# Kernel optimization log

Hardware: AMD Instinct MI355X
Metric: run time of the kernel (lower is better)

Reference implementation:

```python
import jax, jax.numpy as jnp
import numpy as np

NUM_HEADS = 16
HEAD_DIM = 128  # 2048 / 16


def setup_inputs() -> dict:
    key = jax.random.key(0)
    ks = jax.random.split(key, 5)
    B, S, D = 2, 2048, 2048
    scale = 1.0 / np.sqrt(D)
    return {
        "x": jax.random.normal(ks[0], (B, S, D), dtype=jnp.float32),
        "Wq": jax.random.normal(ks[1], (D, D), dtype=jnp.float32) * scale,
        "Wk": jax.random.normal(ks[2], (D, D), dtype=jnp.float32) * scale,
        "Wv": jax.random.normal(ks[3], (D, D), dtype=jnp.float32) * scale,
        "Wo": jax.random.normal(ks[4], (D, D), dtype=jnp.float32) * scale,
    }


def reference(x, Wq, Wk, Wv, Wo):
    B, S, D = x.shape
    H, Hd = NUM_HEADS, HEAD_DIM
    # nn.Linear(bias=False): y = x @ W.T
    q = (x @ Wq.T).reshape(B, S, H, Hd).transpose(0, 2, 1, 3)  # [B,H,S,Hd]
    k = (x @ Wk.T).reshape(B, S, H, Hd).transpose(0, 2, 1, 3)
    v = (x @ Wv.T).reshape(B, S, H, Hd).transpose(0, 2, 1, 3)
    scores = jnp.einsum("bhqd,bhkd->bhqk", q, k) / jnp.sqrt(jnp.float32(Hd))
    attn = jax.nn.softmax(scores, axis=-1)  # dropout p=0 (eval) -> identity
    out = jnp.einsum("bhqk,bhkd->bhqd", attn, v)  # [B,H,S,Hd]
    out = out.transpose(0, 2, 1, 3).reshape(B, S, D)
    out = out @ Wo.T
    return out
```

## Files before the change

### kernel.cpp

```cpp
#include <hip/hip_runtime.h>
#include <math.h>
#include <stdint.h>


#define DDIM 2048
#define SEQ  2048
#define NH   16
#define HD   128

typedef __attribute__((ext_vector_type(4))) float f32x4;
typedef __attribute__((ext_vector_type(16))) float f32x16;
typedef __attribute__((ext_vector_type(8))) __bf16 bf16x8;
typedef __attribute__((ext_vector_type(4))) unsigned int u32x4;
typedef __attribute__((ext_vector_type(2))) unsigned int u32x2;

#define MFMA_B16(a, b, c) __builtin_amdgcn_mfma_f32_16x16x32_bf16((a), (b), (c), 0, 0, 0)
#define MFMA32(a, b, c) __builtin_amdgcn_mfma_f32_32x32x16_bf16((a), (b), (c), 0, 0, 0)

__device__ __forceinline__ void async16(const void* g, void* l) {
  __builtin_amdgcn_global_load_lds(
      (const __attribute__((address_space(1))) unsigned int*)g,
      (__attribute__((address_space(3))) unsigned int*)l, 16, 0, 0);
}

__device__ __forceinline__ unsigned short f2bf(float f) {
  unsigned u = __builtin_bit_cast(unsigned, f);
  u += 0x7fffu + ((u >> 16) & 1u);
  return (unsigned short)(u >> 16);
}

__device__ __forceinline__ bf16x8 ldfrag(const unsigned short* p) {
  return __builtin_bit_cast(bf16x8, *(const u32x4*)p);
}

__device__ __forceinline__ void cvt_body(const float* __restrict__ s,
                                         unsigned short* __restrict__ d, int i) {
  const f32x4* sp = (const f32x4*)s;
  f32x4 a = sp[2 * i], b = sp[2 * i + 1];
  u32x4 o;
  o.x = ((unsigned)f2bf(a.y) << 16) | f2bf(a.x);
  o.y = ((unsigned)f2bf(a.w) << 16) | f2bf(a.z);
  o.z = ((unsigned)f2bf(b.y) << 16) | f2bf(b.x);
  o.w = ((unsigned)f2bf(b.w) << 16) | f2bf(b.z);
  ((u32x4*)d)[i] = o;
}

__global__ __launch_bounds__(256) void cvt_bf16_kernel(const float* __restrict__ s,
                                                       unsigned short* __restrict__ d) {
  cvt_body(s, d, blockIdx.x * 256 + threadIdx.x);
}

__global__ __launch_bounds__(256) void cvt_all_kernel(const float* __restrict__ x,
                                                      const float* __restrict__ wq,
                                                      const float* __restrict__ wk,
                                                      const float* __restrict__ wv,
                                                      const float* __restrict__ wo,
                                                      unsigned short* __restrict__ xb,
                                                      unsigned short* __restrict__ wqkv,
                                                      unsigned short* __restrict__ wob) {
  const int b = blockIdx.x;
  if (b < 4096) {
    cvt_body(x, xb, b * 256 + threadIdx.x);
  } else if (b < 10240) {
    const int wi = (b - 4096) >> 11, lb = (b - 4096) & 2047;
    const float* s = (wi == 0) ? wq : (wi == 1) ? wk : wv;
    cvt_body(s, wqkv + (size_t)wi * 4194304u, lb * 256 + threadIdx.x);
  } else {
    cvt_body(wo, wob, (b - 10240) * 256 + threadIdx.x);
  }
}

#define STG_A(NXT, HOFF, CB)                                              \
  {                                                                       \
    async16(pA[0] + (HOFF) * DDIM + (CB), &As[NXT][(HOFF) * 64 + tid * 8]); \
    async16(pA[1] + (HOFF) * DDIM + (CB),                                 \
            &As[NXT][(HOFF) * 64 + 4096 + tid * 8]);                      \
  }
#define STG_B(NXT, HOFF, CB)                                              \
  {                                                                       \
    async16(pB[0] + (HOFF) * DDIM + (CB), &Bs[NXT][(HOFF) * 64 + tid * 8]); \
    async16(pB[1] + (HOFF) * DDIM + (CB),                                 \
            &Bs[NXT][(HOFF) * 64 + 4096 + tid * 8]);                      \
  }
#define VM0 asm volatile("s_waitcnt vmcnt(0)" ::: "memory")
#define VMNONE (void)0

#define PHASE2(CUR, KS, STAGE_STMT, WAIT_STMT)                        \
  {                                                                   \
    const int ph = (KS) * 2 + half;                                   \
    bf16x8 af_[4], bf_[2];                                            \
    _Pragma("unroll") for (int mf = 0; mf < 4; ++mf) af_[mf] =        \
        ldfrag(&As[CUR][(wr * 128 + mf * 32 + l32) * 64 +             \
                        (ph ^ fr ^ ((mf & 1) * 4)) * 8]);             \
    _Pragma("unroll") for (int nf = 0; nf < 2; ++nf) bf_[nf] =        \
        ldfrag(&Bs[CUR][(wc * 64 + nf * 32 + l32) * 64 +              \
                        (ph ^ fr ^ (nf * 4)) * 8]);                   \
    STAGE_STMT;                                                       \
    __builtin_amdgcn_s_barrier();                                     \
    asm volatile("s_waitcnt lgkmcnt(0)" ::: "memory");                \
    __builtin_amdgcn_sched_barrier(0);                                \
    __builtin_amdgcn_s_setprio(1);                                    \
    _Pragma("unroll") for (int mf = 0; mf < 4; ++mf) {                \
      acc[mf][0] = MFMA32(af_[mf], bf_[0], acc[mf][0]);               \
      acc[mf][1] = MFMA32(af_[mf], bf_[1], acc[mf][1]);               \
    }                                                                 \
    __builtin_amdgcn_s_setprio(0);                                    \
    WAIT_STMT;                                                        \
    __builtin_amdgcn_s_barrier();                                     \
  }

__global__ __launch_bounds__(512) void gemm_qkv8(const unsigned short* __restrict__ A,
                                                 const unsigned short* __restrict__ B,
                                                 unsigned short* __restrict__ Oqk,
                                                 unsigned short* __restrict__ Ovt,
                                                 float alpha_q) {
  __shared__ unsigned short As[2][256 * 64];
  __shared__ unsigned short Bs[2][256 * 64];
  const int tid = threadIdx.x;
  const int lane = tid & 63, w = tid >> 6;
  const int l32 = lane & 31, half = lane >> 5;
  const int wr = w >> 2, wc = w & 3;
  const int bm = blockIdx.y * 256, bn = blockIdx.x * 256;

  const int fr = (l32 & 7) ^ (l32 >> 3);

  f32x16 acc[4][2];
#pragma unroll
  for (int mf = 0; mf < 4; ++mf)
#pragma unroll
    for (int nf = 0; nf < 2; ++nf)
#pragma unroll
      for (int e = 0; e < 16; ++e) acc[mf][nf][e] = 0.f;

  const unsigned short* pA[2];
  const unsigned short* pB[2];
#pragma unroll
  for (int j = 0; j < 2; ++j) {
    const int slot = j * 512 + tid;
    const int rowl = slot >> 3, cs = slot & 7;
    const int g = cs ^ (rowl & 7) ^ ((rowl >> 3) & 7);
    pA[j] = A + (size_t)(bm + rowl) * DDIM + g * 8;
    pB[j] = B + (size_t)(bn + rowl) * DDIM + g * 8;
  }

  STG_A(0, 0, 0);
  STG_A(0, 128, 0);
  STG_B(0, 0, 0);
  STG_B(0, 128, 0);
  asm volatile("s_waitcnt vmcnt(0)" ::: "memory");
  __builtin_amdgcn_s_barrier();

#pragma unroll 1
  for (int kt = 0; kt < 32; ++kt) {
    const int cur = kt & 1, nxt = cur ^ 1;
    const int cb = ((kt + 1) & 31) * 64;
    PHASE2(cur, 0, { STG_A(nxt, 0, cb); STG_A(nxt, 128, cb); }, VMNONE);
    PHASE2(cur, 1, { STG_B(nxt, 0, cb); STG_B(nxt, 128, cb); }, VMNONE);
    PHASE2(cur, 2, VMNONE, VMNONE);
    PHASE2(cur, 3, VMNONE, VM0);
  }

  const int seg = bn >> 11;
  const int bnl = bn & 2047;
  const float alpha = (seg == 0) ? alpha_q : 1.0f;
#pragma unroll
  for (int mf = 0; mf < 4; ++mf) {
#pragma unroll
    for (int nf = 0; nf < 2; ++nf) {
#pragma unroll
      for (int rg = 0; rg < 4; ++rg) {
        const int m0 = bm + wr * 128 + mf * 32 + rg * 8 + half * 4;
        const float v0 = acc[mf][nf][rg * 4 + 0] * alpha;
        const float v1 = acc[mf][nf][rg * 4 + 1] * alpha;
        const float v2 = acc[mf][nf][rg * 4 + 2] * alpha;
        const float v3 = acc[mf][nf][rg * 4 + 3] * alpha;
        const int n = bnl + wc * 64 + nf * 32 + l32;
        if (seg < 2) {
          unsigned short* O = Oqk + (size_t)seg * (4096u * 2048u);
          O[(size_t)(m0 + 0) * DDIM + n] = f2bf(v0);
          O[(size_t)(m0 + 1) * DDIM + n] = f2bf(v1);
          O[(size_t)(m0 + 2) * DDIM + n] = f2bf(v2);
          O[(size_t)(m0 + 3) * DDIM + n] = f2bf(v3);
        } else {
          const int bb = m0 >> 11, s0 = m0 & 2047;
          const int hh = n >> 7, dd = n & 127;
          u32x2 st;
          st.x = ((unsigned)f2bf(v1) << 16) | f2bf(v0);
          st.y = ((unsigned)f2bf(v3) << 16) | f2bf(v2);
          *(u32x2*)&Ovt[((size_t)((bb * NH + hh) * HD + dd)) * SEQ + s0] = st;
        }
      }
    }
  }
}

__global__ __launch_bounds__(256) void gemm_o64(const unsigned short* __restrict__ A,
                                                const unsigned short* __restrict__ B,
                                                float* __restrict__ Cf) {
  __shared__ unsigned short As[128 * 64];
  __shared__ unsigned short Bs[64 * 64];
  const int tid = threadIdx.x;
  const int lane = tid & 63, w = tid >> 6;
  const int l32 = lane & 31, half = lane >> 5;
  const int wm = (w >> 1) * 64, wn = (w & 1) * 32;
  const int bm = blockIdx.y * 128, bn = blockIdx.x * 64;

  f32x16 acc[2];
#pragma unroll
  for (int i = 0; i < 2; ++i)
#pragma unroll
    for (int e = 0; e < 16; ++e) acc[i][e] = 0.f;

  const unsigned short* pa[4];
  const unsigned short* pbb[2];
  {
#pragma unroll
    for (int j = 0; j < 4; ++j) {
      const int row = j * 32 + (tid >> 3);
      const int cg = (tid & 7) ^ (row & 7) ^ ((row >> 3) & 7);
      pa[j] = A + (size_t)(bm + row) * DDIM + cg * 8;
      if (j < 2) pbb[j] = B + (size_t)(bn + row) * DDIM + cg * 8;
    }
  }

  const int fr = (l32 & 7) ^ (l32 >> 3);
  const int fb = fr ^ ((wn >> 3) & 4);

  for (int kt = 0; kt < 32; ++kt) {
    __syncthreads();
#pragma unroll
    for (int j = 0; j < 4; ++j) {
      async16(pa[j], &As[(j * 256 + tid) * 8]);
      pa[j] += 64;
      if (j < 2) {
        async16(pbb[j], &Bs[(j * 256 + tid) * 8]);
        pbb[j] += 64;
      }
    }
    __syncthreads();
#pragma unroll
    for (int ks = 0; ks < 4; ++ks) {
      const int ph = ks * 2 + half;
      bf16x8 af0 = ldfrag(&As[(wm + l32) * 64 + (ph ^ fr) * 8]);
      bf16x8 af1 = ldfrag(&As[(wm + 32 + l32) * 64 + (ph ^ fr ^ 4) * 8]);
      bf16x8 bf0 = ldfrag(&Bs[(wn + l32) * 64 + (ph ^ fb) * 8]);
      acc[0] = MFMA32(af0, bf0, acc[0]);
      acc[1] = MFMA32(af1, bf0, acc[1]);
    }
  }

#pragma unroll
  for (int i = 0; i < 2; ++i) {
#pragma unroll
    for (int rg = 0; rg < 4; ++rg) {
      const int m0 = bm + wm + i * 32 + rg * 8 + half * 4;
      const int n = bn + wn + l32;
      Cf[(size_t)(m0 + 0) * DDIM + n] = acc[i][rg * 4 + 0];
      Cf[(size_t)(m0 + 1) * DDIM + n] = acc[i][rg * 4 + 1];
      Cf[(size_t)(m0 + 2) * DDIM + n] = acc[i][rg * 4 + 2];
      Cf[(size_t)(m0 + 3) * DDIM + n] = acc[i][rg * 4 + 3];
    }
  }
}

__global__ __launch_bounds__(512) void attn_kernel(const unsigned short* __restrict__ qb,
                                                   const unsigned short* __restrict__ kb,
                                                   const unsigned short* __restrict__ vtb,
                                                   unsigned short* __restrict__ ab) {
  __shared__ unsigned short Ks[64 * 128];
  __shared__ unsigned short Vts[128 * 64];
  __shared__ unsigned short Pw[8 * 16 * 40];
  const int tid = threadIdx.x;
  const int w = tid >> 6, lane = tid & 63;
  const int quad = lane >> 4, l16 = lane & 15;
  const int qt = blockIdx.x, bh = blockIdx.y;
  const int b = bh >> 4, h = bh & 15;
  const int qrow = qt * 128 + w * 16 + l16;

  const unsigned short* qp = qb + ((size_t)(b * SEQ + qrow)) * DDIM + h * HD;
  bf16x8 qf[4];
#pragma unroll
  for (int ks = 0; ks < 4; ++ks) qf[ks] = ldfrag(qp + ks * 32 + quad * 8);

  f32x4 ot[8];
#pragma unroll
  for (int i = 0; i < 8; i++) ot[i] = f32x4{0.f, 0.f, 0.f, 0.f};
  float sumacc = 0.f;

  const unsigned short* kp[2];
  const unsigned short* vp[2];
  {
    const size_t kbase = ((size_t)(b * SEQ)) * DDIM + h * HD;
    const size_t vbase = ((size_t)((b * NH + h) * HD)) * SEQ;
#pragma unroll
    for (int j = 0; j < 2; ++j) {
      const int key = j * 32 + (tid >> 4), cgk = (tid & 15) ^ (key & 15);
      kp[j] = kb + kbase + (size_t)key * DDIM + cgk * 8;
      const int dd = j * 64 + (tid >> 3), cgv = (tid & 7) ^ (dd & 7);
      vp[j] = vtb + vbase + (size_t)dd * SEQ + cgv * 8;
    }
  }
  unsigned short* pw = &Pw[w * 640];

  for (int kt = 0; kt < SEQ / 64; ++kt) {
    __syncthreads();
#pragma unroll
    for (int j = 0; j < 2; ++j) {
      async16(kp[j], &Ks[(j * 512 + tid) * 8]);
      kp[j] += (size_t)64 * DDIM;
      async16(vp[j], &Vts[(j * 512 + tid) * 8]);
      vp[j] += 64;
    }
    __syncthreads();
    f32x4 s[4];
#pragma unroll
    for (int t = 0; t < 4; ++t) s[t] = f32x4{0.f, 0.f, 0.f, 0.f};
#pragma unroll
    for (int ks = 0; ks < 4; ++ks) {
      const int sl = ((ks * 4 + quad) ^ l16) * 8;
#pragma unroll
      for (int t = 0; t < 4; ++t) {
        bf16x8 a = ldfrag(&Ks[(t * 16 + l16) * 128 + sl]);
        s[t] = MFMA_B16(a, qf[ks], s[t]);
      }
    }
    f32x4 p[4];
#pragma unroll
    for (int t = 0; t < 4; ++t) {
      p[t].x = __builtin_amdgcn_exp2f(s[t].x);
      p[t].y = __builtin_amdgcn_exp2f(s[t].y);
      p[t].z = __builtin_amdgcn_exp2f(s[t].z);
      p[t].w = __builtin_amdgcn_exp2f(s[t].w);
      sumacc += (p[t].x + p[t].y) + (p[t].z + p[t].w);
    }
    bf16x8 pb0, pb1;
    {
      u32x2 w0, w1;
      w0.x = ((unsigned)f2bf(p[0].y) << 16) | f2bf(p[0].x);
      w0.y = ((unsigned)f2bf(p[0].w) << 16) | f2bf(p[0].z);
      w1.x = ((unsigned)f2bf(p[1].y) << 16) | f2bf(p[1].x);
      w1.y = ((unsigned)f2bf(p[1].w) << 16) | f2bf(p[1].z);
      *(u32x2*)&pw[l16 * 40 + quad * 4] = w0;
      *(u32x2*)&pw[l16 * 40 + 16 + quad * 4] = w1;
      asm volatile("s_waitcnt lgkmcnt(0)" ::: "memory");
      pb0 = ldfrag(&pw[l16 * 40 + quad * 8]);
      w0.x = ((unsigned)f2bf(p[2].y) << 16) | f2bf(p[2].x);
      w0.y = ((unsigned)f2bf(p[2].w) << 16) | f2bf(p[2].z);
      w1.x = ((unsigned)f2bf(p[3].y) << 16) | f2bf(p[3].x);
      w1.y = ((unsigned)f2bf(p[3].w) << 16) | f2bf(p[3].z);
      *(u32x2*)&pw[l16 * 40 + quad * 4] = w0;
      *(u32x2*)&pw[l16 * 40 + 16 + quad * 4] = w1;
      asm volatile("s_waitcnt lgkmcnt(0)" ::: "memory");
      pb1 = ldfrag(&pw[l16 * 40 + quad * 8]);
    }
#pragma unroll
    for (int mt = 0; mt < 8; ++mt) {
      bf16x8 vf0 = ldfrag(&Vts[(mt * 16 + l16) * 64 + (quad ^ (l16 & 7)) * 8]);
      ot[mt] = MFMA_B16(vf0, pb0, ot[mt]);
      bf16x8 vf1 = ldfrag(&Vts[(mt * 16 + l16) * 64 + ((4 + quad) ^ (l16 & 7)) * 8]);
      ot[mt] = MFMA_B16(vf1, pb1, ot[mt]);
    }
  }
  float total = sumacc;
  total += __shfl_xor(total, 16);
  total += __shfl_xor(total, 32);
  const float inv = 1.0f / total;
  unsigned short* op = ab + ((size_t)(b * SEQ + qrow)) * DDIM + h * HD;
#pragma unroll
  for (int mt = 0; mt < 8; ++mt) {
    f32x4 v = ot[mt] * inv;
    u32x2 st;
    st.x = ((unsigned)f2bf(v.y) << 16) | f2bf(v.x);
    st.y = ((unsigned)f2bf(v.w) << 16) | f2bf(v.z);
    *(u32x2*)&op[mt * 16 + quad * 4] = st;
  }
}

extern "C" void kernel_launch(void* const* d_in, const int* in_sizes, int n_in,
                              void* d_out, int out_size, void* d_ws, size_t ws_size,
                              hipStream_t stream) {
  (void)in_sizes; (void)n_in; (void)out_size;
  const float* x = (const float*)d_in[0];
  const float* Wq = (const float*)d_in[1];
  const float* Wk = (const float*)d_in[2];
  const float* Wv = (const float*)d_in[3];
  const float* Wo = (const float*)d_in[4];

  char* ws = (char*)d_ws;
  unsigned short* xb = (unsigned short*)(ws);
  unsigned short* wqkv = (unsigned short*)(ws + 16777216);
  unsigned short* qb = (unsigned short*)(ws + 41943040);
  unsigned short* kb = (unsigned short*)(ws + 58720256);
  unsigned short* vtb = (unsigned short*)(ws + 75497472);
  const bool big = ws_size >= 100663296ull;
  unsigned short* wob = big ? (unsigned short*)(ws + 92274688) : wqkv;

  const float alpha_q = 1.44269504088896341f / sqrtf(128.0f);

  if (big) {
    cvt_all_kernel<<<dim3(12288), 256, 0, stream>>>(x, Wq, Wk, Wv, Wo, xb, wqkv, wob);
    gemm_qkv8<<<dim3(24, 16), 512, 0, stream>>>(xb, wqkv, qb, vtb, alpha_q);
  } else {
    cvt_all_kernel<<<dim3(10240), 256, 0, stream>>>(x, Wq, Wk, Wv, Wo, xb, wqkv, wob);
    gemm_qkv8<<<dim3(24, 16), 512, 0, stream>>>(xb, wqkv, qb, vtb, alpha_q);
    cvt_bf16_kernel<<<dim3(2048), 256, 0, stream>>>(Wo, wob);
  }

  attn_kernel<<<dim3(16, 32), 512, 0, stream>>>(qb, kb, vtb, xb);

  gemm_o64<<<dim3(32, 32), 256, 0, stream>>>(xb, wob, (float*)d_out);
}
```

Measured before the change: 391.6 us.

## Double-buffer LDS fragments in registers and cut barriers in QKV GEMM loop

Rewrites the QKV projection GEMM main loop so that LDS fragment reads for the next k-substep are issued into a second register set while MFMAs run on the current set. Partial lgkmcnt waits replace the full lgkmcnt(0) waits. The per-iteration barrier count drops from eight to two. This is meant to hide LDS read latency behind matrix-core work, at the cost of extra VGPRs for the second fragment set and more delicate cross-wave ordering around buffer reuse.

```diff
diff --git a/kernel.cpp b/kernel.cpp
--- a/kernel.cpp
+++ b/kernel.cpp
@@ -70,44 +70,40 @@
   }
 }
 
-#define STG_A(NXT, HOFF, CB)                                              \
-  {                                                                       \
+#define STG_A(NXT, HOFF, CB)                                                \
+  {                                                                         \
     async16(pA[0] + (HOFF) * DDIM + (CB), &As[NXT][(HOFF) * 64 + tid * 8]); \
-    async16(pA[1] + (HOFF) * DDIM + (CB),                                 \
-            &As[NXT][(HOFF) * 64 + 4096 + tid * 8]);                      \
-  }
-#define STG_B(NXT, HOFF, CB)                                              \
-  {                                                                       \
+    async16(pA[1] + (HOFF) * DDIM + (CB),                                   \
+            &As[NXT][(HOFF) * 64 + 4096 + tid * 8]);                        \
+  }
+#define STG_B(NXT, HOFF, CB)                                                \
+  {                                                                         \
     async16(pB[0] + (HOFF) * DDIM + (CB), &Bs[NXT][(HOFF) * 64 + tid * 8]); \
-    async16(pB[1] + (HOFF) * DDIM + (CB),                                 \
-            &Bs[NXT][(HOFF) * 64 + 4096 + tid * 8]);                      \
-  }
-#define VM0 asm volatile("s_waitcnt vmcnt(0)" ::: "memory")
-#define VMNONE (void)0
-
-#define PHASE2(CUR, KS, STAGE_STMT, WAIT_STMT)                        \
-  {                                                                   \
-    const int ph = (KS) * 2 + half;                                   \
-    bf16x8 af_[4], bf_[2];                                            \
-    _Pragma("unroll") for (int mf = 0; mf < 4; ++mf) af_[mf] =        \
-        ldfrag(&As[CUR][(wr * 128 + mf * 32 + l32) * 64 +             \
-                        (ph ^ fr ^ ((mf & 1) * 4)) * 8]);             \
-    _Pragma("unroll") for (int nf = 0; nf < 2; ++nf) bf_[nf] =        \
-        ldfrag(&Bs[CUR][(wc * 64 + nf * 32 + l32) * 64 +              \
-                        (ph ^ fr ^ (nf * 4)) * 8]);                   \
-    STAGE_STMT;                                                       \
-    __builtin_amdgcn_s_barrier();                                     \
-    asm volatile("s_waitcnt lgkmcnt(0)" ::: "memory");                \
-    __builtin_amdgcn_sched_barrier(0);                                \
-    __builtin_amdgcn_s_setprio(1);                                    \
-    _Pragma("unroll") for (int mf = 0; mf < 4; ++mf) {                \
-      acc[mf][0] = MFMA32(af_[mf], bf_[0], acc[mf][0]);               \
-      acc[mf][1] = MFMA32(af_[mf], bf_[1], acc[mf][1]);               \
-    }                                                                 \
-    __builtin_amdgcn_s_setprio(0);                                    \
-    WAIT_STMT;                                                        \
-    __builtin_amdgcn_s_barrier();                                     \
-  }
+    async16(pB[1] + (HOFF) * DDIM + (CB),                                   \
+            &Bs[NXT][(HOFF) * 64 + 4096 + tid * 8]);                        \
+  }
+
+#define READ6(CUR, KS, FA, FB)                                                    \
+  _Pragma("unroll") for (int mf = 0; mf < 4; ++mf)                                \
+      FA[mf] = ldfrag(&As[CUR][(wr * 128 + mf * 32 + l32) * 64 +                  \
+                               ((((KS) * 2) + half) ^ fr ^ ((mf & 1) * 4)) * 8]); \
+  _Pragma("unroll") for (int nf = 0; nf < 2; ++nf)                                \
+      FB[nf] = ldfrag(&Bs[CUR][(wc * 64 + nf * 32 + l32) * 64 +                   \
+                               ((((KS) * 2) + half) ^ fr ^ (nf * 4)) * 8]);
+
+#define LGKM6                                              \
+  do {                                                     \
+    asm volatile("s_waitcnt lgkmcnt(6)" ::: "memory");     \
+    __builtin_amdgcn_sched_barrier(0);                     \
+  } while (0)
+
+#define MFMA8(FA, FB)                                      \
+  __builtin_amdgcn_s_setprio(1);                           \
+  _Pragma("unroll") for (int mf = 0; mf < 4; ++mf) {       \
+    acc[mf][0] = MFMA32(FA[mf], FB[0], acc[mf][0]);        \
+    acc[mf][1] = MFMA32(FA[mf], FB[1], acc[mf][1]);        \
+  }                                                        \
+  __builtin_amdgcn_s_setprio(0);
 
 __global__ __launch_bounds__(512) void gemm_qkv8(const unsigned short* __restrict__ A,
                                                  const unsigned short* __restrict__ B,
@@ -132,6 +128,8 @@
 #pragma unroll
       for (int e = 0; e < 16; ++e) acc[mf][nf][e] = 0.f;
 
+  bf16x8 fXa[4], fXb[2], fYa[4], fYb[2];
+
   const unsigned short* pA[2];
   const unsigned short* pB[2];
 #pragma unroll
@@ -149,16 +147,33 @@
   STG_B(0, 128, 0);
   asm volatile("s_waitcnt vmcnt(0)" ::: "memory");
   __builtin_amdgcn_s_barrier();
+  READ6(0, 0, fXa, fXb);
 
 #pragma unroll 1
   for (int kt = 0; kt < 32; ++kt) {
     const int cur = kt & 1, nxt = cur ^ 1;
     const int cb = ((kt + 1) & 31) * 64;
-    PHASE2(cur, 0, { STG_A(nxt, 0, cb); STG_A(nxt, 128, cb); }, VMNONE);
-    PHASE2(cur, 1, { STG_B(nxt, 0, cb); STG_B(nxt, 128, cb); }, VMNONE);
-    PHASE2(cur, 2, VMNONE, VMNONE);
-    PHASE2(cur, 3, VMNONE, VM0);
-  }
+    READ6(cur, 1, fYa, fYb);
+    STG_A(nxt, 0, cb);
+    STG_A(nxt, 128, cb);
+    LGKM6;
+    MFMA8(fXa, fXb);
+    READ6(cur, 2, fXa, fXb);
+    STG_B(nxt, 0, cb);
+    STG_B(nxt, 128, cb);
+    LGKM6;
+    MFMA8(fYa, fYb);
+    READ6(cur, 3, fYa, fYb);
+    LGKM6;
+    MFMA8(fXa, fXb);
+    asm volatile("s_waitcnt vmcnt(0)" ::: "memory");
+    __builtin_amdgcn_s_barrier();
+    READ6(nxt, 0, fXa, fXb);
+    LGKM6;
+    MFMA8(fYa, fYb);
+    __builtin_amdgcn_s_barrier();
+  }
+  asm volatile("s_waitcnt vmcnt(0) lgkmcnt(0)" ::: "memory");
 
   const int seg = bn >> 11;
   const int bnl = bn & 2047;
```

After: 388.4 us. No clear change (-0.8%).
